# Optimization experiments

Measured on AMD Instinct MI355X. Metric: run time of the kernel, lower is better.

The kernel has to match this reference:

```python
import jax, jax.numpy as jnp
import numpy as np

DIM = 256
HID = DIM * 16

def setup_inputs() -> dict:
    key = jax.random.key(0)
    ks = jax.random.split(key, 6)
    B, L = 4, 2048
    x = jax.random.normal(ks[0], (B, L, DIM), dtype=jnp.float32)
    # nn.Linear(dim, hidden): weight [H, D], bias [H]
    WB = jax.random.normal(ks[1], (HID, DIM), dtype=jnp.float32) / np.sqrt(DIM)
    bB = jax.random.normal(ks[2], (HID,), dtype=jnp.float32) * 0.01
    # nn.Linear(hidden, dim): weight [D, H], bias [D]
    WC = jax.random.normal(ks[3], (DIM, HID), dtype=jnp.float32) / np.sqrt(HID)
    bC = jax.random.normal(ks[4], (DIM,), dtype=jnp.float32) * 0.01
    A = jax.random.normal(ks[5], (HID,), dtype=jnp.float32)
    return {"x": x, "WB": WB, "bB": bB, "WC": WC, "bC": bC, "A": A}

def reference(x, WB, bB, WC, bC, A):
    # b = B(x): [B, L, H]
    b = jnp.einsum('bld,hd->blh', x, WB) + bB
    a = jax.nn.sigmoid(A)  # [H], time-invariant decay
    # h_t = a * h_{t-1} + b_t  (h_0 from zero state) -> associative scan over L
    a_seq = jnp.broadcast_to(a, b.shape)
    def comb(c1, c2):
        a1, u1 = c1
        a2, u2 = c2
        return (a1 * a2, a2 * u1 + u2)
    _, h = jax.lax.associative_scan(comb, (a_seq, b), axis=1)  # [B, L, H]
    # C(h): [B, L, D]
    return jnp.einsum('blh,dh->bld', h, WC) + bC
```

## Files before the change

### kernel.cpp

```cpp
#include <hip/hip_runtime.h>
#include <hip/hip_bf16.h>

#define DIMSZ 256
#define HID 4096
#define BATCH 4
#define SEQ 2048
#define NCH 64
#define CLEN 32
#define SPLITK2 4
#define KCHUNK (HID / SPLITK2)
#define BM2 64

typedef __bf16 bf16_t;
typedef __bf16 bf16x4 __attribute__((ext_vector_type(4)));
typedef __bf16 bf16x8 __attribute__((ext_vector_type(8)));
typedef float  f32x4  __attribute__((ext_vector_type(4)));

__device__ __forceinline__ float sigmoidf_dev(float x) {
    return 1.0f / (1.0f + __expf(-x));
}

__device__ __forceinline__ bf16x8 cvt8(const float* p) {
    bf16x8 o;
    #pragma unroll
    for (int j = 0; j < 8; j++) o[j] = (bf16_t)p[j];
    return o;
}

__global__ void prep_kernel(const float* __restrict__ x,
                            const float* __restrict__ WB,
                            const float* __restrict__ WC,
                            bf16_t* __restrict__ xt,
                            bf16_t* __restrict__ WBt,
                            bf16_t* __restrict__ Wt) {
    int i = blockIdx.x * blockDim.x + threadIdx.x;
    if (i < 262144) {
        int lane = i & 63, m16 = (i >> 6) & 511, ks = i >> 15;
        int row = m16 * 16 + (lane & 15);
        int k   = ks * 32 + (lane >> 4) * 8;
        *(bf16x8*)&xt[(size_t)i * 8] = cvt8(&x[(size_t)row * DIMSZ + k]);
    } else if (i < 393216) {
        int j = i - 262144;
        int lane = j & 63, n16 = (j >> 6) & 255, ks = j >> 14;
        int row = n16 * 16 + (lane & 15);
        int k   = ks * 32 + (lane >> 4) * 8;
        *(bf16x8*)&WBt[(size_t)j * 8] = cvt8(&WB[(size_t)row * DIMSZ + k]);
    } else {
        int j = i - 393216;
        int lane = j & 63, g = (j >> 6) & 15, ks = j >> 10;
        int row = g * 16 + (lane & 15);
        int k   = ks * 32 + (lane >> 4) * 8;
        *(bf16x8*)&Wt[(size_t)j * 8] = cvt8(&WC[(size_t)row * HID + k]);
    }
}

__global__ __launch_bounds__(256)
void gemm1_fused(const bf16_t* __restrict__ xt, const bf16_t* __restrict__ WBt,
                 const float* __restrict__ bias, const float* __restrict__ Adecay,
                 bf16_t* __restrict__ Cg, float* __restrict__ totals)
{
    constexpr int LDT = 136;
    __shared__ bf16_t tile[128 * LDT];

    const int tid = threadIdx.x, wave = tid >> 6, lane = tid & 63;
    const int wm = wave >> 1, wn = wave & 1, q = lane >> 4, r16 = lane & 15;
    const int mBase = blockIdx.x * 128, nBase = blockIdx.y * 128;
    const int m16Base = blockIdx.x * 8 + wm * 4;
    const int n16Base = blockIdx.y * 8 + wn * 4;
    const int batch = mBase >> 11, tIn = mBase & 2047;
    const int cg0 = tIn >> 5;

    f32x4 acc[4][4] = {};

    #pragma unroll 2
    for (int ks = 0; ks < 8; ks++) {
        bf16x8 af[4], bfr[4];
        #pragma unroll
        for (int mt = 0; mt < 4; mt++)
            af[mt] = *(const bf16x8*)&xt[(((size_t)ks * 512 + m16Base + mt) * 64 + lane) * 8];
        #pragma unroll
        for (int nt = 0; nt < 4; nt++)
            bfr[nt] = *(const bf16x8*)&WBt[(((size_t)ks * 256 + n16Base + nt) * 64 + lane) * 8];
        #pragma unroll
        for (int mt = 0; mt < 4; mt++)
            #pragma unroll
            for (int nt = 0; nt < 4; nt++)
                acc[mt][nt] = __builtin_amdgcn_mfma_f32_16x16x32_bf16(
                    af[mt], bfr[nt], acc[mt][nt], 0, 0, 0);
    }

    #pragma unroll
    for (int nt = 0; nt < 4; nt++) {
        const int chl = wn * 64 + nt * 16 + r16;
        const float bv = bias[nBase + chl];
        #pragma unroll
        for (int mt = 0; mt < 4; mt++) {
            const int t0 = wm * 64 + mt * 16 + q * 4;
            bf16x4 pk;
            #pragma unroll
            for (int rg = 0; rg < 4; rg++)
                pk[rg] = (bf16_t)(acc[mt][nt][rg] + bv);
            *(bf16x4*)&tile[chl * LDT + t0] = pk;
        }
    }
    __syncthreads();

    #pragma unroll
    for (int p = 0; p < 8; p++) {
        const int cc = p >> 1;
        const int tt = (p & 1) * 256 + tid;
        const int ch = tt >> 2, oo = tt & 3;
        *(bf16x8*)&Cg[((size_t)(batch * NCH + cg0 + cc) * HID + nBase + ch) * 32 + oo * 8] =
            *(const bf16x8*)&tile[ch * LDT + cc * 32 + oo * 8];
    }

    #pragma unroll
    for (int t = 0; t < 2; t++) {
        const int task = tid + t * 256;
        const int ch = task & 127, ck = task >> 7;
        const float a = sigmoidf_dev(Adecay[nBase + ch]);
        float tot = 0.f;
        #pragma unroll
        for (int o = 0; o < 4; o++) {
            bf16x8 v8 = *(const bf16x8*)&tile[ch * LDT + ck * CLEN + o * 8];
            #pragma unroll
            for (int j = 0; j < 8; j++)
                tot = a * tot + (float)v8[j];
        }
        totals[(size_t)(batch * NCH + cg0 + ck) * HID + nBase + ch] = tot;
    }
}

__global__ void scan_carries_kernel(const float* __restrict__ totals,
                                    const float* __restrict__ Adecay,
                                    float* __restrict__ carries)
{
    int gid = blockIdx.x * 64 + threadIdx.x;
    int ch    = gid & (HID - 1);
    int batch = gid >> 12;
    float a = sigmoidf_dev(Adecay[ch]);
    float aC = a;
    #pragma unroll
    for (int i = 0; i < 5; i++) aC *= aC;

    float v[NCH];
    #pragma unroll
    for (int c = 0; c < NCH; c++)
        v[c] = totals[(size_t)(batch * NCH + c) * HID + ch];

    float carry = 0.f;
    #pragma unroll
    for (int c = 0; c < NCH; c++) {
        carries[(size_t)(batch * NCH + c) * HID + ch] = carry;
        carry = aC * carry + v[c];
    }
}

__global__ __launch_bounds__(256, 2)
void gemm2_fused(const bf16_t* __restrict__ bv, const bf16_t* __restrict__ Wt,
                 const float* __restrict__ Adecay, const float* __restrict__ carries,
                 bf16_t* __restrict__ P)
{
    constexpr int CKSTRIDE = CLEN * 32 + 32;
    constexpr int CHOFF = 8 * CKSTRIDE;
    __shared__ bf16_t hs[2][2 * CHOFF];

    const int tid = threadIdx.x, wave = tid >> 6, lane = tid & 63;
    const int q = lane >> 4, r16 = lane & 15;
    const int mBase = blockIdx.x * BM2;
    const int kBase = blockIdx.y * KCHUNK;
    const int batch = mBase >> 11, tIn = mBase & 2047;
    const int chunk0 = tIn >> 5;

    const size_t base0 = ((size_t)(batch * NCH + chunk0) * HID + kBase + tid) * 32;
    const size_t base1 = base0 + (size_t)HID * 32;

    bf16x8 rA[8], rB[8];

    #define LOAD_SLAB(R, S)                                                   \
        do {                                                                  \
            _Pragma("unroll")                                                 \
            for (int o = 0; o < 4; o++) {                                     \
                R[o]     = *(const bf16x8*)&bv[base0 + (S) * 8192 + o * 8];   \
                R[4 + o] = *(const bf16x8*)&bv[base1 + (S) * 8192 + o * 8];   \
            }                                                                 \
        } while (0)

    LOAD_SLAB(rA, 0);

    float aD[4], sd0[4], sd1[4];
    #pragma unroll
    for (int s = 0; s < 4; s++) {
        const int c = kBase + s * 256 + tid;
        aD[s]  = Adecay[c];
        sd0[s] = carries[(size_t)(batch * NCH + chunk0) * HID + c];
        sd1[s] = carries[(size_t)(batch * NCH + chunk0 + 1) * HID + c];
    }

    LOAD_SLAB(rB, 1);

    f32x4 acc[2][2][4] = {};

    #define SCAN_SLAB(R, S, PG)                                               \
        do {                                                                  \
            const float a = sigmoidf_dev(aD[S]);                              \
            float st0 = sd0[S], st1 = sd1[S];                                 \
            bf16_t* hw0 = &hs[PG][(tid >> 5) * CKSTRIDE];                     \
            bf16_t* hw1 = hw0 + CHOFF;                                        \
            const int cho = (tid >> 3) & 3, chi = tid & 7;                    \
            _Pragma("unroll")                                                 \
            for (int o = 0; o < 4; o++) {                                     \
                _Pragma("unroll")                                             \
                for (int j = 0; j < 8; j++) {                                 \
                    const int t = o * 8 + j;                                  \
                    const int sw = t * 32 + ((cho ^ ((t >> 2) & 3)) << 3) + chi; \
                    st0 = a * st0 + (float)R[o][j];                           \
                    hw0[sw] = (bf16_t)st0;                                    \
                    st1 = a * st1 + (float)R[4 + o][j];                       \
                    hw1[sw] = (bf16_t)st1;                                    \
                }                                                             \
            }                                                                 \
        } while (0)

    auto mfma_phase = [&](const bf16_t* hb, int s) {
        const int ksBase = (kBase >> 5) + s * 8;
        #pragma unroll 2
        for (int cki = 0; cki < 8; cki++) {
            bf16x8 af[2][2], bfr[4];
            #pragma unroll
            for (int nt = 0; nt < 4; nt++)
                bfr[nt] = *(const bf16x8*)&Wt[
                    (((size_t)(ksBase + cki) * 16 + wave * 4 + nt) * 64 + lane) * 8];
            #pragma unroll
            for (int c = 0; c < 2; c++)
                #pragma unroll
                for (int mt = 0; mt < 2; mt++)
                    af[c][mt] = *(const bf16x8*)&hb[c * CHOFF + cki * CKSTRIDE
                                 + (mt * 16 + r16) * 32 + ((q ^ (r16 >> 2)) << 3)];
            #pragma unroll
            for (int c = 0; c < 2; c++)
                #pragma unroll
                for (int mt = 0; mt < 2; mt++)
                    #pragma unroll
                    for (int nt = 0; nt < 4; nt++)
                        acc[c][mt][nt] = __builtin_amdgcn_mfma_f32_16x16x32_bf16(
                            af[c][mt], bfr[nt], acc[c][mt][nt], 0, 0, 0);
        }
    };

    SCAN_SLAB(rA, 0, 0);
    __syncthreads();

    LOAD_SLAB(rA, 2);
    SCAN_SLAB(rB, 1, 1);
    mfma_phase(&hs[0][0], 0);
    __syncthreads();

    LOAD_SLAB(rB, 3);
    SCAN_SLAB(rA, 2, 0);
    mfma_phase(&hs[1][0], 1);
    __syncthreads();

    SCAN_SLAB(rB, 3, 1);
    mfma_phase(&hs[0][0], 2);
    __syncthreads();

    mfma_phase(&hs[1][0], 3);
    #pragma unroll
    for (int nt = 0; nt < 4; nt++) {
        const int col = wave * 64 + nt * 16 + r16;
        #pragma unroll
        for (int c = 0; c < 2; c++)
            #pragma unroll
            for (int mt = 0; mt < 2; mt++)
                #pragma unroll
                for (int rg = 0; rg < 4; rg++)
                    hs[0][(c * 32 + mt * 16 + q * 4 + rg) * 264 + col] =
                        (bf16_t)acc[c][mt][nt][rg];
    }
    __syncthreads();

    bf16_t* Pb = P + (size_t)blockIdx.y * (BATCH * SEQ) * DIMSZ;
    #pragma unroll
    for (int p = 0; p < 8; p++) {
        const int task = p * 256 + tid;
        const int r = task >> 5, g8 = (task & 31) << 3;
        *(bf16x8*)&Pb[(size_t)(mBase + r) * DIMSZ + g8] =
            *(const bf16x8*)&hs[0][r * 264 + g8];
    }
    #undef LOAD_SLAB
    #undef SCAN_SLAB
}

__global__ void reduce_out_kernel(const bf16_t* __restrict__ P,
                                  const float* __restrict__ bias,
                                  float* __restrict__ out, int nTask) {
    int i = blockIdx.x * blockDim.x + threadIdx.x;
    if (i >= nTask) return;
    int n8 = (i & 31) << 3;
    size_t off = (size_t)i * 8;
    float v[8];
    #pragma unroll
    for (int j = 0; j < 8; j++) v[j] = bias[n8 + j];
    #pragma unroll
    for (int sp = 0; sp < SPLITK2; sp++) {
        bf16x8 p = *(const bf16x8*)&P[(size_t)sp * (BATCH * SEQ) * DIMSZ + off];
        #pragma unroll
        for (int j = 0; j < 8; j++) v[j] += (float)p[j];
    }
    float4* o4 = (float4*)&out[off];
    o4[0] = make_float4(v[0], v[1], v[2], v[3]);
    o4[1] = make_float4(v[4], v[5], v[6], v[7]);
}

extern "C" void kernel_launch(void* const* d_in, const int* in_sizes, int n_in,
                              void* d_out, int out_size, void* d_ws, size_t ws_size,
                              hipStream_t stream)
{
    const float* x  = (const float*)d_in[0];
    const float* WB = (const float*)d_in[1];
    const float* bB = (const float*)d_in[2];
    const float* WC = (const float*)d_in[3];
    const float* bC = (const float*)d_in[4];
    const float* A  = (const float*)d_in[5];

    char* ws = (char*)d_ws;
    size_t off = 0;
    bf16_t* xt   = (bf16_t*)(ws + off); off += (size_t)BATCH * SEQ * DIMSZ * 2;
    bf16_t* WBt  = (bf16_t*)(ws + off); off += (size_t)HID * DIMSZ * 2;
    bf16_t* Wt   = (bf16_t*)(ws + off); off += (size_t)DIMSZ * HID * 2;
    bf16_t* bbuf = (bf16_t*)(ws + off); off += (size_t)BATCH * SEQ * HID * 2;
    bf16_t* partials = (bf16_t*)(ws + off); off += (size_t)SPLITK2 * BATCH * SEQ * DIMSZ * 2;
    float* totals   = (float*)(ws + off); off += (size_t)BATCH * NCH * HID * 4;
    float* carries  = (float*)(ws + off); off += (size_t)BATCH * NCH * HID * 4;

    const int M = BATCH * SEQ;

    prep_kernel<<<2048, 256, 0, stream>>>(x, WB, WC, xt, WBt, Wt);

    dim3 g1(M / 128, HID / 128);
    gemm1_fused<<<g1, 256, 0, stream>>>(xt, WBt, bB, A, bbuf, totals);

    scan_carries_kernel<<<256, 64, 0, stream>>>(totals, A, carries);

    dim3 g2(M / BM2, SPLITK2);
    gemm2_fused<<<g2, 256, 0, stream>>>(bbuf, Wt, A, carries, partials);

    int nTask = M * DIMSZ / 8;
    reduce_out_kernel<<<(nTask + 255) / 256, 256, 0, stream>>>(
        partials, bC, (float*)d_out, nTask);
}
```

Baseline: 139.6 us.

## Double gemm2 block to 512 threads, splitting chunks across wave groups

The fused scan+GEMM2 kernel now runs 512 threads per block instead of 256. Each half of the block scans one of the two time chunks, and each wave computes a 32-row MFMA tile instead of two. This halves per-thread registers and serial scan work and adds waves to hide latency. The cost is that both wave groups now load the same Wt fragments, and launch bounds ask for higher occupancy, which may limit registers.

```diff
diff --git a/kernel.cpp b/kernel.cpp
--- a/kernel.cpp
+++ b/kernel.cpp
@@ -156,7 +156,7 @@
     }
 }
 
-__global__ __launch_bounds__(256, 2)
+__global__ __launch_bounds__(512, 4)
 void gemm2_fused(const bf16_t* __restrict__ bv, const bf16_t* __restrict__ Wt,
                  const float* __restrict__ Adecay, const float* __restrict__ carries,
                  bf16_t* __restrict__ P)
@@ -172,79 +172,73 @@
     const int batch = mBase >> 11, tIn = mBase & 2047;
     const int chunk0 = tIn >> 5;
 
-    const size_t base0 = ((size_t)(batch * NCH + chunk0) * HID + kBase + tid) * 32;
-    const size_t base1 = base0 + (size_t)HID * 32;
-
-    bf16x8 rA[8], rB[8];
+    const int ck2 = tid >> 8, ch = tid & 255;
+
+    const size_t base = ((size_t)(batch * NCH + chunk0 + ck2) * HID + kBase + ch) * 32;
+
+    bf16x8 rA[4], rB[4];
 
     #define LOAD_SLAB(R, S)                                                   \
         do {                                                                  \
             _Pragma("unroll")                                                 \
-            for (int o = 0; o < 4; o++) {                                     \
-                R[o]     = *(const bf16x8*)&bv[base0 + (S) * 8192 + o * 8];   \
-                R[4 + o] = *(const bf16x8*)&bv[base1 + (S) * 8192 + o * 8];   \
-            }                                                                 \
+            for (int o = 0; o < 4; o++)                                       \
+                R[o] = *(const bf16x8*)&bv[base + (S) * 8192 + o * 8];        \
         } while (0)
 
     LOAD_SLAB(rA, 0);
 
-    float aD[4], sd0[4], sd1[4];
+    float aD[4], sd[4];
     #pragma unroll
     for (int s = 0; s < 4; s++) {
-        const int c = kBase + s * 256 + tid;
-        aD[s]  = Adecay[c];
-        sd0[s] = carries[(size_t)(batch * NCH + chunk0) * HID + c];
-        sd1[s] = carries[(size_t)(batch * NCH + chunk0 + 1) * HID + c];
+        const int c = kBase + s * 256 + ch;
+        aD[s] = Adecay[c];
+        sd[s] = carries[(size_t)(batch * NCH + chunk0 + ck2) * HID + c];
     }
 
     LOAD_SLAB(rB, 1);
 
-    f32x4 acc[2][2][4] = {};
+    f32x4 acc[2][4] = {};
 
     #define SCAN_SLAB(R, S, PG)                                               \
         do {                                                                  \
             const float a = sigmoidf_dev(aD[S]);                              \
-            float st0 = sd0[S], st1 = sd1[S];                                 \
-            bf16_t* hw0 = &hs[PG][(tid >> 5) * CKSTRIDE];                     \
-            bf16_t* hw1 = hw0 + CHOFF;                                        \
-            const int cho = (tid >> 3) & 3, chi = tid & 7;                    \
+            float st = sd[S];                                                 \
+            bf16_t* hw = &hs[PG][ck2 * CHOFF + (ch >> 5) * CKSTRIDE];         \
+            const int cho = (ch >> 3) & 3, chi = ch & 7;                      \
             _Pragma("unroll")                                                 \
             for (int o = 0; o < 4; o++) {                                     \
                 _Pragma("unroll")                                             \
                 for (int j = 0; j < 8; j++) {                                 \
                     const int t = o * 8 + j;                                  \
-                    const int sw = t * 32 + ((cho ^ ((t >> 2) & 3)) << 3) + chi; \
-                    st0 = a * st0 + (float)R[o][j];                           \
-                    hw0[sw] = (bf16_t)st0;                                    \
-                    st1 = a * st1 + (float)R[4 + o][j];                       \
-                    hw1[sw] = (bf16_t)st1;                                    \
+                    st = a * st + (float)R[o][j];                             \
+                    hw[t * 32 + ((cho ^ ((t >> 2) & 3)) << 3) + chi] = (bf16_t)st; \
                 }                                                             \
             }                                                                 \
         } while (0)
 
+    const int wc = wave >> 2;
+    const int wn = wave & 3;
+
     auto mfma_phase = [&](const bf16_t* hb, int s) {
         const int ksBase = (kBase >> 5) + s * 8;
+        const bf16_t* hbc = hb + wc * CHOFF;
         #pragma unroll 2
         for (int cki = 0; cki < 8; cki++) {
-            bf16x8 af[2][2], bfr[4];
+            bf16x8 af[2], bfr[4];
             #pragma unroll
             for (int nt = 0; nt < 4; nt++)
                 bfr[nt] = *(const bf16x8*)&Wt[
-                    (((size_t)(ksBase + cki) * 16 + wave * 4 + nt) * 64 + lane) * 8];
-            #pragma unroll
-            for (int c = 0; c < 2; c++)
+                    (((size_t)(ksBase + cki) * 16 + wn * 4 + nt) * 64 + lane) * 8];
+            #pragma unroll
+            for (int mt = 0; mt < 2; mt++)
+                af[mt] = *(const bf16x8*)&hbc[cki * CKSTRIDE + (mt * 16 + r16) * 32
+                                              + ((q ^ (r16 >> 2)) << 3)];
+            #pragma unroll
+            for (int mt = 0; mt < 2; mt++)
                 #pragma unroll
-                for (int mt = 0; mt < 2; mt++)
-                    af[c][mt] = *(const bf16x8*)&hb[c * CHOFF + cki * CKSTRIDE
-                                 + (mt * 16 + r16) * 32 + ((q ^ (r16 >> 2)) << 3)];
-            #pragma unroll
-            for (int c = 0; c < 2; c++)
-                #pragma unroll
-                for (int mt = 0; mt < 2; mt++)
-                    #pragma unroll
-                    for (int nt = 0; nt < 4; nt++)
-                        acc[c][mt][nt] = __builtin_amdgcn_mfma_f32_16x16x32_bf16(
-                            af[c][mt], bfr[nt], acc[c][mt][nt], 0, 0, 0);
+                for (int nt = 0; nt < 4; nt++)
+                    acc[mt][nt] = __builtin_amdgcn_mfma_f32_16x16x32_bf16(
+                        af[mt], bfr[nt], acc[mt][nt], 0, 0, 0);
         }
     };
 
@@ -268,22 +262,20 @@
     mfma_phase(&hs[1][0], 3);
     #pragma unroll
     for (int nt = 0; nt < 4; nt++) {
-        const int col = wave * 64 + nt * 16 + r16;
-        #pragma unroll
-        for (int c = 0; c < 2; c++)
-            #pragma unroll
-            for (int mt = 0; mt < 2; mt++)
-                #pragma unroll
-                for (int rg = 0; rg < 4; rg++)
-                    hs[0][(c * 32 + mt * 16 + q * 4 + rg) * 264 + col] =
-                        (bf16_t)acc[c][mt][nt][rg];
+        const int col = wn * 64 + nt * 16 + r16;
+        #pragma unroll
+        for (int mt = 0; mt < 2; mt++)
+            #pragma unroll
+            for (int rg = 0; rg < 4; rg++)
+                hs[0][(wc * 32 + mt * 16 + q * 4 + rg) * 264 + col] =
+                    (bf16_t)acc[mt][nt][rg];
     }
     __syncthreads();
 
     bf16_t* Pb = P + (size_t)blockIdx.y * (BATCH * SEQ) * DIMSZ;
     #pragma unroll
-    for (int p = 0; p < 8; p++) {
-        const int task = p * 256 + tid;
+    for (int p = 0; p < 4; p++) {
+        const int task = p * 512 + tid;
         const int r = task >> 5, g8 = (task & 31) << 3;
         *(bf16x8*)&Pb[(size_t)(mBase + r) * DIMSZ + g8] =
             *(const bf16x8*)&hs[0][r * 264 + g8];
@@ -344,7 +336,7 @@
     scan_carries_kernel<<<256, 64, 0, stream>>>(totals, A, carries);
 
     dim3 g2(M / BM2, SPLITK2);
-    gemm2_fused<<<g2, 256, 0, stream>>>(bbuf, Wt, A, carries, partials);
+    gemm2_fused<<<g2, 512, 0, stream>>>(bbuf, Wt, A, carries, partials);
 
     int nTask = M * DIMSZ / 8;
     reduce_out_kernel<<<(nTask + 255) / 256, 256, 0, stream>>>(
```

New measurement: 140.4 us. About the same (+0.6%).

## Double-buffer GEMM1 operand tiles in LDS via direct global-to-LDS loads

Applied to the files above, without the earlier changes.

Operand fragments for the first GEMM are no longer read by each wave straight from global memory. The block now stages each K-slice of x and WB into a double-buffered LDS tile using global_load_lds, and the next slice is prefetched while MFMAs run on the current one. The goal is to stop waves that share rows or columns from fetching the same global data twice, and to overlap load latency with compute. In exchange it adds a barrier per K step and relies on the barrier also waiting for the asynchronous LDS loads to finish.

```diff
diff --git a/kernel.cpp b/kernel.cpp
--- a/kernel.cpp
+++ b/kernel.cpp
@@ -18,6 +18,13 @@
 
 __device__ __forceinline__ float sigmoidf_dev(float x) {
     return 1.0f / (1.0f + __expf(-x));
+}
+
+__device__ __forceinline__ void load_lds16(const bf16_t* g, bf16_t* l) {
+    __builtin_amdgcn_global_load_lds(
+        (const __attribute__((address_space(1))) void*)g,
+        (__attribute__((address_space(3))) void*)l,
+        16, 0, 0);
 }
 
 __device__ __forceinline__ bf16x8 cvt8(const float* p) {
@@ -65,29 +72,44 @@
     const int tid = threadIdx.x, wave = tid >> 6, lane = tid & 63;
     const int wm = wave >> 1, wn = wave & 1, q = lane >> 4, r16 = lane & 15;
     const int mBase = blockIdx.x * 128, nBase = blockIdx.y * 128;
-    const int m16Base = blockIdx.x * 8 + wm * 4;
-    const int n16Base = blockIdx.y * 8 + wn * 4;
     const int batch = mBase >> 11, tIn = mBase & 2047;
     const int cg0 = tIn >> 5;
 
+    auto stage = [&](int ks, int buf) {
+        #pragma unroll
+        for (int i = 0; i < 2; i++) {
+            const int g = wave * 2 + i;
+            load_lds16(&xt[(((size_t)ks * 512 + blockIdx.x * 8 + g) * 64 + lane) * 8],
+                       &tile[buf * 8192 + g * 512]);
+            load_lds16(&WBt[(((size_t)ks * 256 + blockIdx.y * 8 + g) * 64 + lane) * 8],
+                       &tile[buf * 8192 + 4096 + g * 512]);
+        }
+    };
+
+    stage(0, 0);
+
     f32x4 acc[4][4] = {};
-
-    #pragma unroll 2
+    int cur = 0;
+    #pragma unroll
     for (int ks = 0; ks < 8; ks++) {
+        __syncthreads();
+        if (ks < 7) stage(ks + 1, cur ^ 1);
         bf16x8 af[4], bfr[4];
         #pragma unroll
         for (int mt = 0; mt < 4; mt++)
-            af[mt] = *(const bf16x8*)&xt[(((size_t)ks * 512 + m16Base + mt) * 64 + lane) * 8];
+            af[mt] = *(const bf16x8*)&tile[cur * 8192 + (wm * 4 + mt) * 512 + lane * 8];
         #pragma unroll
         for (int nt = 0; nt < 4; nt++)
-            bfr[nt] = *(const bf16x8*)&WBt[(((size_t)ks * 256 + n16Base + nt) * 64 + lane) * 8];
+            bfr[nt] = *(const bf16x8*)&tile[cur * 8192 + 4096 + (wn * 4 + nt) * 512 + lane * 8];
         #pragma unroll
         for (int mt = 0; mt < 4; mt++)
             #pragma unroll
             for (int nt = 0; nt < 4; nt++)
                 acc[mt][nt] = __builtin_amdgcn_mfma_f32_16x16x32_bf16(
                     af[mt], bfr[nt], acc[mt][nt], 0, 0, 0);
-    }
+        cur ^= 1;
+    }
+    __syncthreads();
 
     #pragma unroll
     for (int nt = 0; nt < 4; nt++) {
```

Result: no change. 137.4 us (-1.6%).
